# Optimization experiments

Hardware: AMD Instinct MI355X
Metric: run time of the kernel (lower is better)

The kernel has to match this reference:

```python
import jax, jax.numpy as jnp
import numpy as np

NUM_GRAPHS = 128

def setup_inputs() -> dict:
    key = jax.random.key(0)
    k1, k2, k3, k4, k5, k6 = jax.random.split(key, 6)
    N, E, H = 100000, 3200000, 256
    x = jax.random.normal(k1, (N, 1), dtype=jnp.float32)
    edge_index = jax.random.randint(k2, (2, E), 0, N, dtype=jnp.int64)
    batch = jnp.sort(jax.random.randint(k3, (N,), 0, NUM_GRAPHS, dtype=jnp.int64))
    # SAGEConv lin_l: [in=1 -> out=H], plus bias; final Linear [H -> 1]
    W_l = jax.random.normal(k4, (1, H), dtype=jnp.float32) / jnp.sqrt(1.0)
    b_l = jnp.zeros((H,), dtype=jnp.float32)
    W_out = jax.random.normal(k5, (H, 1), dtype=jnp.float32) / jnp.sqrt(H)
    b_out = jax.random.normal(k6, (1,), dtype=jnp.float32) * 0.01
    return {"x": x, "edge_index": edge_index, "batch": batch,
            "W_l": W_l, "b_l": b_l, "W_out": W_out, "b_out": b_out}

def reference(x, edge_index, batch, W_l, b_l, W_out, b_out):
    N = x.shape[0]
    src, dst = edge_index[0], edge_index[1]
    # SAGEConv(aggr='sum', root_weight=False): agg[i] = sum_{j->i} x[j]; out = agg @ W_l + b_l
    agg = jax.ops.segment_sum(x[src], dst, num_segments=N)  # [N,1]
    h = agg @ W_l + b_l                                      # [N,H]
    h = jax.nn.relu(h)
    # global_mean_pool over batch ids
    sums = jax.ops.segment_sum(h, batch, num_segments=NUM_GRAPHS)          # [G,H]
    counts = jax.ops.segment_sum(jnp.ones((N,), h.dtype), batch, num_segments=NUM_GRAPHS)
    pooled = sums / jnp.maximum(counts, 1.0)[:, None]
    out = pooled @ W_out + b_out                             # [G,1]
    return jax.nn.relu(out)
```

## Files before the change

kernel.cpp:

```cpp
#include <hip/hip_runtime.h>


#define GMAX  128
#define HMAX  256
#define BS    256
#define NBMAX 512
#define SG    512
#define BLK2  512
#define CEDGE 6400
#define RSTR  16


__global__ __launch_bounds__(BLK2) void s2_sort(const int* __restrict__ ei,
                                                unsigned* __restrict__ grank,
                                                unsigned* __restrict__ pairs,
                                                int E, int NB, int QpB, int CAP) {
  __shared__ unsigned lp[CEDGE];
  __shared__ unsigned short lb[CEDGE];
  __shared__ unsigned hist[NBMAX];
  __shared__ unsigned sc[NBMAX];
  __shared__ unsigned lbase[NBMAX];
  __shared__ unsigned lrank[NBMAX];
  __shared__ unsigned hb[NBMAX];
  int tid = threadIdx.x, blk = blockIdx.x;

  for (int b = tid; b < NBMAX; b += BLK2) { hist[b] = 0u; lrank[b] = 0u; }
  __syncthreads();

  int Q = E >> 2;
  int q0 = blk * QpB;
  int q1 = min(q0 + QpB, Q);
  const int4* s4 = (const int4*)ei;
  const int4* d4 = (const int4*)(ei + E);

  for (int q = q0 + tid; q < q1; q += BLK2) {
    int4 d = d4[q];
    atomicAdd(&hist[d.x >> 8], 1u);
    atomicAdd(&hist[d.y >> 8], 1u);
    atomicAdd(&hist[d.z >> 8], 1u);
    atomicAdd(&hist[d.w >> 8], 1u);
  }
  if (blk == 0)
    for (int e = (Q << 2) + tid; e < E; e += BLK2)
      atomicAdd(&hist[ei[E + e] >> 8], 1u);
  __syncthreads();

  for (int b = tid; b < NBMAX; b += BLK2) sc[b] = hist[b];
  __syncthreads();
  for (int o = 1; o < NBMAX; o <<= 1) {
    unsigned v = 0u;
    if (tid < NBMAX && tid >= o) v = sc[tid - o];
    __syncthreads();
    if (tid < NBMAX) sc[tid] += v;
    __syncthreads();
  }
  for (int b = tid; b < NB; b += BLK2) {
    unsigned c = hist[b];
    lbase[b] = sc[b] - c;
    unsigned r = c ? atomicAdd(&grank[(size_t)b * RSTR], c) : 0u;
    hb[b] = (unsigned)b * (unsigned)CAP + r;
  }
  __syncthreads();

  for (int q = q0 + tid; q < q1; q += BLK2) {
    int4 s = s4[q];
    int4 d = d4[q];
    { int b = d.x >> 8; unsigned r = atomicAdd(&lrank[b], 1u);
      unsigned p = lbase[b] + r;
      lp[p] = ((unsigned)s.x << 8) | (unsigned)(d.x & 255); lb[p] = (unsigned short)b; }
    { int b = d.y >> 8; unsigned r = atomicAdd(&lrank[b], 1u);
      unsigned p = lbase[b] + r;
      lp[p] = ((unsigned)s.y << 8) | (unsigned)(d.y & 255); lb[p] = (unsigned short)b; }
    { int b = d.z >> 8; unsigned r = atomicAdd(&lrank[b], 1u);
      unsigned p = lbase[b] + r;
      lp[p] = ((unsigned)s.z << 8) | (unsigned)(d.z & 255); lb[p] = (unsigned short)b; }
    { int b = d.w >> 8; unsigned r = atomicAdd(&lrank[b], 1u);
      unsigned p = lbase[b] + r;
      lp[p] = ((unsigned)s.w << 8) | (unsigned)(d.w & 255); lb[p] = (unsigned short)b; }
  }
  int total = (q1 - q0) * 4;
  if (blk == 0) {
    for (int e = (Q << 2) + tid; e < E; e += BLK2) {
      int d = ei[E + e], s = ei[e];
      int b = d >> 8; unsigned r = atomicAdd(&lrank[b], 1u);
      unsigned p = lbase[b] + r;
      lp[p] = ((unsigned)s << 8) | (unsigned)(d & 255); lb[p] = (unsigned short)b;
    }
    total += (E & 3);
  }
  if (total > CEDGE) total = CEDGE;
  __syncthreads();

  unsigned capu = (unsigned)CAP;
  for (int i = tid; i < total; i += BLK2) {
    unsigned b = lb[i];
    unsigned slot = hb[b] + ((unsigned)i - lbase[b]);
    if (slot < (b + 1u) * capu)
      pairs[slot] = lp[i];
  }
}

__global__ __launch_bounds__(1024) void s3_reduce(
    const unsigned* __restrict__ pairs, const unsigned* __restrict__ grank,
    const float* __restrict__ x, const int* __restrict__ batch,
    const float* __restrict__ Wl, const float* __restrict__ bl,
    const float* __restrict__ Wo, const float* __restrict__ b_out,
    float* __restrict__ gsum, float* __restrict__ gcnt,
    unsigned* __restrict__ done, float* __restrict__ out,
    int N, int H, int G, int CAP) {
  __shared__ float acc[BS];
  __shared__ float sWl[HMAX], sbl[HMAX], sWo[HMAX];
  __shared__ float ls[GMAX], lc[GMAX];
  __shared__ unsigned ticket;
  int tid = threadIdx.x, b = blockIdx.x;
  if (tid < BS) acc[tid] = 0.f;
  if (tid < H) { sWl[tid] = Wl[tid]; sbl[tid] = bl[tid]; sWo[tid] = Wo[tid]; }
  if (tid < GMAX) { ls[tid] = 0.f; lc[tid] = 0.f; }
  __syncthreads();

  unsigned lo = (unsigned)b * (unsigned)CAP;
  unsigned cnt = min(grank[(size_t)b * RSTR], (unsigned)CAP);
  unsigned q4 = cnt >> 2;
  const uint4* p4 = (const uint4*)(pairs + lo);
  for (unsigned i = tid; i < q4; i += 1024) {
    uint4 p = p4[i];
    atomicAdd(&acc[p.x & 255u], x[p.x >> 8]);
    atomicAdd(&acc[p.y & 255u], x[p.y >> 8]);
    atomicAdd(&acc[p.z & 255u], x[p.z >> 8]);
    atomicAdd(&acc[p.w & 255u], x[p.w >> 8]);
  }
  if (tid < (int)(cnt & 3u)) {
    unsigned p = pairs[lo + (q4 << 2) + tid];
    atomicAdd(&acc[p & 255u], x[p >> 8]);
  }
  __syncthreads();

  int node = b * BS + tid;
  if (tid < BS && node < N) {
    float a = acc[tid], f = 0.f;
#pragma unroll 8
    for (int k = 0; k < H; ++k) {
      float hh = fmaf(a, sWl[k], sbl[k]);
      f = fmaf(fmaxf(hh, 0.f), sWo[k], f);
    }
    int g = batch[node];
    atomicAdd(&ls[g], f);
    atomicAdd(&lc[g], 1.f);
  }
  __syncthreads();
  if (tid < GMAX && lc[tid] != 0.f) {
    atomicAdd(&gsum[tid], ls[tid]);
    atomicAdd(&gcnt[tid], lc[tid]);
  }
  __syncthreads();
  if (tid == 0)
    ticket = __hip_atomic_fetch_add(done, 1u, __ATOMIC_ACQ_REL,
                                    __HIP_MEMORY_SCOPE_AGENT);
  __syncthreads();
  if (ticket == gridDim.x - 1 && tid < G) {
    float s = __hip_atomic_load(&gsum[tid], __ATOMIC_RELAXED, __HIP_MEMORY_SCOPE_AGENT);
    float c = __hip_atomic_load(&gcnt[tid], __ATOMIC_RELAXED, __HIP_MEMORY_SCOPE_AGENT);
    out[tid] = fmaxf(s / fmaxf(c, 1.f) + b_out[0], 0.f);
  }
}


__global__ __launch_bounds__(256) void fb_scatter(const int* __restrict__ ei,
                                                  const float* __restrict__ x,
                                                  float* __restrict__ agg, int E) {
  int t = blockIdx.x * blockDim.x + threadIdx.x;
  if (t < E) atomicAdd(&agg[ei[E + t]], x[ei[t]]);
}

__global__ __launch_bounds__(256) void fb_node(const float* __restrict__ agg,
                                               const int* __restrict__ batch,
                                               const float* __restrict__ Wl,
                                               const float* __restrict__ bl,
                                               const float* __restrict__ Wo,
                                               float* __restrict__ gsum,
                                               float* __restrict__ gcnt, int N, int H) {
  __shared__ float sWl[HMAX], sbl[HMAX], sWo[HMAX];
  __shared__ float ls[GMAX], lc[GMAX];
  int tid = threadIdx.x;
  if (tid < H) { sWl[tid] = Wl[tid]; sbl[tid] = bl[tid]; sWo[tid] = Wo[tid]; }
  if (tid < GMAX) { ls[tid] = 0.f; lc[tid] = 0.f; }
  __syncthreads();
  int i = blockIdx.x * blockDim.x + tid;
  if (i < N) {
    float a = agg[i], f = 0.f;
    for (int k = 0; k < H; ++k) {
      float hh = fmaf(a, sWl[k], sbl[k]);
      f = fmaf(fmaxf(hh, 0.f), sWo[k], f);
    }
    int g = batch[i];
    atomicAdd(&ls[g], f);
    atomicAdd(&lc[g], 1.f);
  }
  __syncthreads();
  if (tid < GMAX && lc[tid] != 0.f) {
    atomicAdd(&gsum[tid], ls[tid]);
    atomicAdd(&gcnt[tid], lc[tid]);
  }
}

__global__ void fb_final(const float* __restrict__ gsum,
                         const float* __restrict__ gcnt,
                         const float* __restrict__ b_out,
                         float* __restrict__ out, int G) {
  int g = blockIdx.x * blockDim.x + threadIdx.x;
  if (g < G) out[g] = fmaxf(gsum[g] / fmaxf(gcnt[g], 1.f) + b_out[0], 0.f);
}


extern "C" void kernel_launch(void* const* d_in, const int* in_sizes, int n_in,
                              void* d_out, int out_size, void* d_ws, size_t ws_size,
                              hipStream_t stream) {
  const float* x     = (const float*)d_in[0];
  const int*   ei    = (const int*)d_in[1];
  const int*   batch = (const int*)d_in[2];
  const float* Wl    = (const float*)d_in[3];
  const float* bl    = (const float*)d_in[4];
  const float* Wo    = (const float*)d_in[5];
  const float* bo    = (const float*)d_in[6];
  float* out = (float*)d_out;

  int N = in_sizes[0];
  int E = in_sizes[1] / 2;
  int H = in_sizes[3];
  int G = out_size;

  int NB = (N + BS - 1) / BS;
  int Q   = E >> 2;
  int QpB = (Q + SG - 1) / SG;

  int avg = (NB > 0) ? E / NB : 0;
  int CAP = (2 * avg + 4095) & ~4095;
  if (CAP < 4096) CAP = 4096;

  const size_t HDRW = (size_t)NBMAX * RSTR + 2 * GMAX + 4;
  size_t need = (HDRW + (size_t)NB * (size_t)CAP) * 4u;

  unsigned* w = (unsigned*)d_ws;
  if (NB <= NBMAX && ws_size >= need && H <= HMAX && G <= GMAX &&
      QpB * 4 + 4 <= CEDGE) {
    unsigned* grank = w;
    float*    gsum  = (float*)(grank + (size_t)NBMAX * RSTR);
    float*    gcnt  = gsum + GMAX;
    unsigned* done  = (unsigned*)(gcnt + GMAX);
    unsigned* pairs = done + 4;

    hipMemsetAsync(d_ws, 0, HDRW * 4u, stream);
    s2_sort<<<SG, BLK2, 0, stream>>>(ei, grank, pairs, E, NB, QpB, CAP);
    s3_reduce<<<NB, 1024, 0, stream>>>(pairs, grank, x, batch, Wl, bl, Wo, bo,
                                       gsum, gcnt, done, out, N, H, G, CAP);
  } else {
    float* agg  = (float*)d_ws;
    float* gsum = agg + N;
    float* gcnt = gsum + GMAX;
    hipMemsetAsync(d_ws, 0, ((size_t)N + 2 * GMAX) * 4u, stream);
    fb_scatter<<<(E + 255) / 256, 256, 0, stream>>>(ei, x, agg, E);
    fb_node<<<(N + 255) / 256, 256, 0, stream>>>(agg, batch, Wl, bl, Wo,
                                                 gsum, gcnt, N, H);
    fb_final<<<1, 256, 0, stream>>>(gsum, gcnt, bo, out, G);
  }
}
```

Before: 135.8 us.

## Replace bucket-sort aggregation with direct global atomic scatter plus node kernel

Drops the two-pass bucket sort (local histogram, scan, packed pair writes) and shared-memory per-bucket reduction. Edges are now scattered with vectorized int4 loads straight into a global agg array using float atomics, followed by a per-node MLP/pool kernel that keeps the last-block ticket finalize. This removes the pairs write and readback traffic and the sorting work. In exchange, 3.2M edges go through global atomics on random addresses, which may contend or serialize at L2.

```diff
diff --git a/kernel.cpp b/kernel.cpp
--- a/kernel.cpp
+++ b/kernel.cpp
@@ -3,147 +3,53 @@
 
 #define GMAX  128
 #define HMAX  256
-#define BS    256
-#define NBMAX 512
-#define SG    512
-#define BLK2  512
-#define CEDGE 6400
-#define RSTR  16
 
-
-__global__ __launch_bounds__(BLK2) void s2_sort(const int* __restrict__ ei,
-                                                unsigned* __restrict__ grank,
-                                                unsigned* __restrict__ pairs,
-                                                int E, int NB, int QpB, int CAP) {
-  __shared__ unsigned lp[CEDGE];
-  __shared__ unsigned short lb[CEDGE];
-  __shared__ unsigned hist[NBMAX];
-  __shared__ unsigned sc[NBMAX];
-  __shared__ unsigned lbase[NBMAX];
-  __shared__ unsigned lrank[NBMAX];
-  __shared__ unsigned hb[NBMAX];
-  int tid = threadIdx.x, blk = blockIdx.x;
-
-  for (int b = tid; b < NBMAX; b += BLK2) { hist[b] = 0u; lrank[b] = 0u; }
-  __syncthreads();
-
+__global__ __launch_bounds__(256) void e_scatter(const int* __restrict__ ei,
+                                                 const float* __restrict__ x,
+                                                 float* __restrict__ agg, int E) {
   int Q = E >> 2;
-  int q0 = blk * QpB;
-  int q1 = min(q0 + QpB, Q);
   const int4* s4 = (const int4*)ei;
   const int4* d4 = (const int4*)(ei + E);
-
-  for (int q = q0 + tid; q < q1; q += BLK2) {
-    int4 d = d4[q];
-    atomicAdd(&hist[d.x >> 8], 1u);
-    atomicAdd(&hist[d.y >> 8], 1u);
-    atomicAdd(&hist[d.z >> 8], 1u);
-    atomicAdd(&hist[d.w >> 8], 1u);
-  }
-  if (blk == 0)
-    for (int e = (Q << 2) + tid; e < E; e += BLK2)
-      atomicAdd(&hist[ei[E + e] >> 8], 1u);
-  __syncthreads();
-
-  for (int b = tid; b < NBMAX; b += BLK2) sc[b] = hist[b];
-  __syncthreads();
-  for (int o = 1; o < NBMAX; o <<= 1) {
-    unsigned v = 0u;
-    if (tid < NBMAX && tid >= o) v = sc[tid - o];
-    __syncthreads();
-    if (tid < NBMAX) sc[tid] += v;
-    __syncthreads();
-  }
-  for (int b = tid; b < NB; b += BLK2) {
-    unsigned c = hist[b];
-    lbase[b] = sc[b] - c;
-    unsigned r = c ? atomicAdd(&grank[(size_t)b * RSTR], c) : 0u;
-    hb[b] = (unsigned)b * (unsigned)CAP + r;
-  }
-  __syncthreads();
-
-  for (int q = q0 + tid; q < q1; q += BLK2) {
+  int stride = gridDim.x * blockDim.x;
+  for (int q = blockIdx.x * blockDim.x + threadIdx.x; q < Q; q += stride) {
     int4 s = s4[q];
     int4 d = d4[q];
-    { int b = d.x >> 8; unsigned r = atomicAdd(&lrank[b], 1u);
-      unsigned p = lbase[b] + r;
-      lp[p] = ((unsigned)s.x << 8) | (unsigned)(d.x & 255); lb[p] = (unsigned short)b; }
-    { int b = d.y >> 8; unsigned r = atomicAdd(&lrank[b], 1u);
-      unsigned p = lbase[b] + r;
-      lp[p] = ((unsigned)s.y << 8) | (unsigned)(d.y & 255); lb[p] = (unsigned short)b; }
-    { int b = d.z >> 8; unsigned r = atomicAdd(&lrank[b], 1u);
-      unsigned p = lbase[b] + r;
-      lp[p] = ((unsigned)s.z << 8) | (unsigned)(d.z & 255); lb[p] = (unsigned short)b; }
-    { int b = d.w >> 8; unsigned r = atomicAdd(&lrank[b], 1u);
-      unsigned p = lbase[b] + r;
-      lp[p] = ((unsigned)s.w << 8) | (unsigned)(d.w & 255); lb[p] = (unsigned short)b; }
+    float vx = x[s.x], vy = x[s.y], vz = x[s.z], vw = x[s.w];
+    atomicAdd(&agg[d.x], vx);
+    atomicAdd(&agg[d.y], vy);
+    atomicAdd(&agg[d.z], vz);
+    atomicAdd(&agg[d.w], vw);
   }
-  int total = (q1 - q0) * 4;
-  if (blk == 0) {
-    for (int e = (Q << 2) + tid; e < E; e += BLK2) {
-      int d = ei[E + e], s = ei[e];
-      int b = d >> 8; unsigned r = atomicAdd(&lrank[b], 1u);
-      unsigned p = lbase[b] + r;
-      lp[p] = ((unsigned)s << 8) | (unsigned)(d & 255); lb[p] = (unsigned short)b;
-    }
-    total += (E & 3);
-  }
-  if (total > CEDGE) total = CEDGE;
-  __syncthreads();
-
-  unsigned capu = (unsigned)CAP;
-  for (int i = tid; i < total; i += BLK2) {
-    unsigned b = lb[i];
-    unsigned slot = hb[b] + ((unsigned)i - lbase[b]);
-    if (slot < (b + 1u) * capu)
-      pairs[slot] = lp[i];
+  if (blockIdx.x == 0) {
+    for (int e = (Q << 2) + threadIdx.x; e < E; e += 256)
+      atomicAdd(&agg[ei[E + e]], x[ei[e]]);
   }
 }
 
-__global__ __launch_bounds__(1024) void s3_reduce(
-    const unsigned* __restrict__ pairs, const unsigned* __restrict__ grank,
-    const float* __restrict__ x, const int* __restrict__ batch,
+__global__ __launch_bounds__(256) void n_node(
+    const float* __restrict__ agg, const int* __restrict__ batch,
     const float* __restrict__ Wl, const float* __restrict__ bl,
     const float* __restrict__ Wo, const float* __restrict__ b_out,
     float* __restrict__ gsum, float* __restrict__ gcnt,
     unsigned* __restrict__ done, float* __restrict__ out,
-    int N, int H, int G, int CAP) {
-  __shared__ float acc[BS];
+    int N, int H, int G) {
   __shared__ float sWl[HMAX], sbl[HMAX], sWo[HMAX];
   __shared__ float ls[GMAX], lc[GMAX];
   __shared__ unsigned ticket;
-  int tid = threadIdx.x, b = blockIdx.x;
-  if (tid < BS) acc[tid] = 0.f;
+  int tid = threadIdx.x;
   if (tid < H) { sWl[tid] = Wl[tid]; sbl[tid] = bl[tid]; sWo[tid] = Wo[tid]; }
   if (tid < GMAX) { ls[tid] = 0.f; lc[tid] = 0.f; }
   __syncthreads();
 
-  unsigned lo = (unsigned)b * (unsigned)CAP;
-  unsigned cnt = min(grank[(size_t)b * RSTR], (unsigned)CAP);
-  unsigned q4 = cnt >> 2;
-  const uint4* p4 = (const uint4*)(pairs + lo);
-  for (unsigned i = tid; i < q4; i += 1024) {
-    uint4 p = p4[i];
-    atomicAdd(&acc[p.x & 255u], x[p.x >> 8]);
-    atomicAdd(&acc[p.y & 255u], x[p.y >> 8]);
-    atomicAdd(&acc[p.z & 255u], x[p.z >> 8]);
-    atomicAdd(&acc[p.w & 255u], x[p.w >> 8]);
-  }
-  if (tid < (int)(cnt & 3u)) {
-    unsigned p = pairs[lo + (q4 << 2) + tid];
-    atomicAdd(&acc[p & 255u], x[p >> 8]);
-  }
-  __syncthreads();
-
-  int node = b * BS + tid;
-  if (tid < BS && node < N) {
-    float a = acc[tid], f = 0.f;
+  int i = blockIdx.x * blockDim.x + tid;
+  if (i < N) {
+    float a = agg[i], f = 0.f;
 #pragma unroll 8
     for (int k = 0; k < H; ++k) {
       float hh = fmaf(a, sWl[k], sbl[k]);
       f = fmaf(fmaxf(hh, 0.f), sWo[k], f);
     }
-    int g = batch[node];
+    int g = batch[i];
     atomicAdd(&ls[g], f);
     atomicAdd(&lc[g], 1.f);
   }
@@ -165,53 +71,6 @@
 }
 
 
-__global__ __launch_bounds__(256) void fb_scatter(const int* __restrict__ ei,
-                                                  const float* __restrict__ x,
-                                                  float* __restrict__ agg, int E) {
-  int t = blockIdx.x * blockDim.x + threadIdx.x;
-  if (t < E) atomicAdd(&agg[ei[E + t]], x[ei[t]]);
-}
-
-__global__ __launch_bounds__(256) void fb_node(const float* __restrict__ agg,
-                                               const int* __restrict__ batch,
-                                               const float* __restrict__ Wl,
-                                               const float* __restrict__ bl,
-                                               const float* __restrict__ Wo,
-                                               float* __restrict__ gsum,
-                                               float* __restrict__ gcnt, int N, int H) {
-  __shared__ float sWl[HMAX], sbl[HMAX], sWo[HMAX];
-  __shared__ float ls[GMAX], lc[GMAX];
-  int tid = threadIdx.x;
-  if (tid < H) { sWl[tid] = Wl[tid]; sbl[tid] = bl[tid]; sWo[tid] = Wo[tid]; }
-  if (tid < GMAX) { ls[tid] = 0.f; lc[tid] = 0.f; }
-  __syncthreads();
-  int i = blockIdx.x * blockDim.x + tid;
-  if (i < N) {
-    float a = agg[i], f = 0.f;
-    for (int k = 0; k < H; ++k) {
-      float hh = fmaf(a, sWl[k], sbl[k]);
-      f = fmaf(fmaxf(hh, 0.f), sWo[k], f);
-    }
-    int g = batch[i];
-    atomicAdd(&ls[g], f);
-    atomicAdd(&lc[g], 1.f);
-  }
-  __syncthreads();
-  if (tid < GMAX && lc[tid] != 0.f) {
-    atomicAdd(&gsum[tid], ls[tid]);
-    atomicAdd(&gcnt[tid], lc[tid]);
-  }
-}
-
-__global__ void fb_final(const float* __restrict__ gsum,
-                         const float* __restrict__ gcnt,
-                         const float* __restrict__ b_out,
-                         float* __restrict__ out, int G) {
-  int g = blockIdx.x * blockDim.x + threadIdx.x;
-  if (g < G) out[g] = fmaxf(gsum[g] / fmaxf(gcnt[g], 1.f) + b_out[0], 0.f);
-}
-
-
 extern "C" void kernel_launch(void* const* d_in, const int* in_sizes, int n_in,
                               void* d_out, int out_size, void* d_ws, size_t ws_size,
                               hipStream_t stream) {
@@ -229,38 +88,20 @@
   int H = in_sizes[3];
   int G = out_size;
 
-  int NB = (N + BS - 1) / BS;
-  int Q   = E >> 2;
-  int QpB = (Q + SG - 1) / SG;
+  float*    agg  = (float*)d_ws;
+  float*    gsum = agg + N;
+  float*    gcnt = gsum + GMAX;
+  unsigned* done = (unsigned*)(gcnt + GMAX);
 
-  int avg = (NB > 0) ? E / NB : 0;
-  int CAP = (2 * avg + 4095) & ~4095;
-  if (CAP < 4096) CAP = 4096;
+  hipMemsetAsync(d_ws, 0, ((size_t)N + 2 * GMAX + 4) * 4u, stream);
 
-  const size_t HDRW = (size_t)NBMAX * RSTR + 2 * GMAX + 4;
-  size_t need = (HDRW + (size_t)NB * (size_t)CAP) * 4u;
+  int Q = E >> 2;
+  int sg = (Q + 255) / 256;
+  if (sg > 2048) sg = 2048;
+  if (sg < 1) sg = 1;
+  e_scatter<<<sg, 256, 0, stream>>>(ei, x, agg, E);
 
-  unsigned* w = (unsigned*)d_ws;
-  if (NB <= NBMAX && ws_size >= need && H <= HMAX && G <= GMAX &&
-      QpB * 4 + 4 <= CEDGE) {
-    unsigned* grank = w;
-    float*    gsum  = (float*)(grank + (size_t)NBMAX * RSTR);
-    float*    gcnt  = gsum + GMAX;
-    unsigned* done  = (unsigned*)(gcnt + GMAX);
-    unsigned* pairs = done + 4;
-
-    hipMemsetAsync(d_ws, 0, HDRW * 4u, stream);
-    s2_sort<<<SG, BLK2, 0, stream>>>(ei, grank, pairs, E, NB, QpB, CAP);
-    s3_reduce<<<NB, 1024, 0, stream>>>(pairs, grank, x, batch, Wl, bl, Wo, bo,
-                                       gsum, gcnt, done, out, N, H, G, CAP);
-  } else {
-    float* agg  = (float*)d_ws;
-    float* gsum = agg + N;
-    float* gcnt = gsum + GMAX;
-    hipMemsetAsync(d_ws, 0, ((size_t)N + 2 * GMAX) * 4u, stream);
-    fb_scatter<<<(E + 255) / 256, 256, 0, stream>>>(ei, x, agg, E);
-    fb_node<<<(N + 255) / 256, 256, 0, stream>>>(agg, batch, Wl, bl, Wo,
-                                                 gsum, gcnt, N, H);
-    fb_final<<<1, 256, 0, stream>>>(gsum, gcnt, bo, out, G);
-  }
+  int nb = (N + 255) / 256;
+  n_node<<<nb, 256, 0, stream>>>(agg, batch, Wl, bl, Wo, bo,
+                                 gsum, gcnt, done, out, N, H, G);
 }
```

After: 259.1 us. +90.8%, slower.

## Fuse sort and reduce into one cooperative kernel with deterministic bucket offsets

Applied to the files above, without the earlier changes.

Merges the bucketing and reduction kernels into a single cooperative launch that uses grid-wide syncs. Global atomic bucket ranks are replaced by a per-block count matrix whose column prefix sums give each block's offsets. The header zeroing is folded in, which removes the memset. The node MLP loop is split across two half-blocks. This drops two launches and the memset, at the cost of three grid barriers, a hipOccupancy query on every call, and a reduce phase that now runs with 512 threads instead of 1024.

```diff
diff --git a/kernel.cpp b/kernel.cpp
--- a/kernel.cpp
+++ b/kernel.cpp
@@ -1,20 +1,27 @@
 #include <hip/hip_runtime.h>
+#include <hip/hip_cooperative_groups.h>
+
+namespace cg = cooperative_groups;
 
 
 #define GMAX  128
 #define HMAX  256
 #define BS    256
 #define NBMAX 512
-#define SG    512
-#define BLK2  512
+#define NG    512
+#define BLKT  512
 #define CEDGE 6400
-#define RSTR  16
-
-
-__global__ __launch_bounds__(BLK2) void s2_sort(const int* __restrict__ ei,
-                                                unsigned* __restrict__ grank,
-                                                unsigned* __restrict__ pairs,
-                                                int E, int NB, int QpB, int CAP) {
+
+__global__ __launch_bounds__(BLKT, 4) void fused(
+    const int* __restrict__ ei, const float* __restrict__ x,
+    const int* __restrict__ batch, const float* __restrict__ Wl,
+    const float* __restrict__ bl, const float* __restrict__ Wo,
+    const float* __restrict__ bo,
+    unsigned* __restrict__ cnt, unsigned* __restrict__ off,
+    unsigned* __restrict__ tot, float* __restrict__ gsum,
+    float* __restrict__ gcnt, unsigned* __restrict__ done,
+    unsigned* __restrict__ pairs, float* __restrict__ out,
+    int N, int E, int H, int G, int NB, int QpB, int CAP) {
   __shared__ unsigned lp[CEDGE];
   __shared__ unsigned short lb[CEDGE];
   __shared__ unsigned hist[NBMAX];
@@ -22,9 +29,15 @@
   __shared__ unsigned lbase[NBMAX];
   __shared__ unsigned lrank[NBMAX];
   __shared__ unsigned hb[NBMAX];
+  __shared__ float sWl[HMAX], sbl[HMAX], sWo[HMAX];
+  __shared__ float ls[GMAX], lc[GMAX], acc[BS];
+  __shared__ unsigned ticket;
+
+  cg::grid_group grid = cg::this_grid();
   int tid = threadIdx.x, blk = blockIdx.x;
-
-  for (int b = tid; b < NBMAX; b += BLK2) { hist[b] = 0u; lrank[b] = 0u; }
+  int ngrid = (int)gridDim.x;
+
+  for (int b = tid; b < NBMAX; b += BLKT) { hist[b] = 0u; lrank[b] = 0u; }
   __syncthreads();
 
   int Q = E >> 2;
@@ -33,7 +46,7 @@
   const int4* s4 = (const int4*)ei;
   const int4* d4 = (const int4*)(ei + E);
 
-  for (int q = q0 + tid; q < q1; q += BLK2) {
+  for (int q = q0 + tid; q < q1; q += BLKT) {
     int4 d = d4[q];
     atomicAdd(&hist[d.x >> 8], 1u);
     atomicAdd(&hist[d.y >> 8], 1u);
@@ -41,11 +54,11 @@
     atomicAdd(&hist[d.w >> 8], 1u);
   }
   if (blk == 0)
-    for (int e = (Q << 2) + tid; e < E; e += BLK2)
+    for (int e = (Q << 2) + tid; e < E; e += BLKT)
       atomicAdd(&hist[ei[E + e] >> 8], 1u);
   __syncthreads();
 
-  for (int b = tid; b < NBMAX; b += BLK2) sc[b] = hist[b];
+  for (int b = tid; b < NBMAX; b += BLKT) sc[b] = hist[b];
   __syncthreads();
   for (int o = 1; o < NBMAX; o <<= 1) {
     unsigned v = 0u;
@@ -54,15 +67,39 @@
     if (tid < NBMAX) sc[tid] += v;
     __syncthreads();
   }
-  for (int b = tid; b < NB; b += BLK2) {
-    unsigned c = hist[b];
-    lbase[b] = sc[b] - c;
-    unsigned r = c ? atomicAdd(&grank[(size_t)b * RSTR], c) : 0u;
-    hb[b] = (unsigned)b * (unsigned)CAP + r;
-  }
-  __syncthreads();
-
-  for (int q = q0 + tid; q < q1; q += BLK2) {
+  for (int b = tid; b < NBMAX; b += BLKT) lbase[b] = sc[b] - hist[b];
+  for (int b = tid; b < NB; b += BLKT)
+    cnt[(size_t)blk * NBMAX + b] = hist[b];
+  if (blk == ngrid - 1) {
+    if (tid < GMAX) {
+      __hip_atomic_store(&gsum[tid], 0.f, __ATOMIC_RELAXED, __HIP_MEMORY_SCOPE_AGENT);
+      __hip_atomic_store(&gcnt[tid], 0.f, __ATOMIC_RELAXED, __HIP_MEMORY_SCOPE_AGENT);
+    }
+    if (tid == 0)
+      __hip_atomic_store(done, 0u, __ATOMIC_RELAXED, __HIP_MEMORY_SCOPE_AGENT);
+  }
+  grid.sync();
+
+  if (blk < NB) {
+    unsigned c = (tid < ngrid) ? cnt[(size_t)tid * NBMAX + blk] : 0u;
+    sc[tid] = c;
+    __syncthreads();
+    for (int o = 1; o < BLKT; o <<= 1) {
+      unsigned v = (tid >= o) ? sc[tid - o] : 0u;
+      __syncthreads();
+      sc[tid] += v;
+      __syncthreads();
+    }
+    if (tid < ngrid) off[(size_t)tid * NBMAX + blk] = sc[tid] - c;
+    if (tid == BLKT - 1) tot[blk] = sc[tid];
+  }
+  grid.sync();
+
+  for (int b = tid; b < NB; b += BLKT)
+    hb[b] = (unsigned)b * (unsigned)CAP + off[(size_t)blk * NBMAX + b];
+  __syncthreads();
+
+  for (int q = q0 + tid; q < q1; q += BLKT) {
     int4 s = s4[q];
     int4 d = d4[q];
     { int b = d.x >> 8; unsigned r = atomicAdd(&lrank[b], 1u);
@@ -80,7 +117,7 @@
   }
   int total = (q1 - q0) * 4;
   if (blk == 0) {
-    for (int e = (Q << 2) + tid; e < E; e += BLK2) {
+    for (int e = (Q << 2) + tid; e < E; e += BLKT) {
       int d = ei[E + e], s = ei[e];
       int b = d >> 8; unsigned r = atomicAdd(&lrank[b], 1u);
       unsigned p = lbase[b] + r;
@@ -92,60 +129,58 @@
   __syncthreads();
 
   unsigned capu = (unsigned)CAP;
-  for (int i = tid; i < total; i += BLK2) {
+  for (int i = tid; i < total; i += BLKT) {
     unsigned b = lb[i];
     unsigned slot = hb[b] + ((unsigned)i - lbase[b]);
     if (slot < (b + 1u) * capu)
       pairs[slot] = lp[i];
   }
-}
-
-__global__ __launch_bounds__(1024) void s3_reduce(
-    const unsigned* __restrict__ pairs, const unsigned* __restrict__ grank,
-    const float* __restrict__ x, const int* __restrict__ batch,
-    const float* __restrict__ Wl, const float* __restrict__ bl,
-    const float* __restrict__ Wo, const float* __restrict__ b_out,
-    float* __restrict__ gsum, float* __restrict__ gcnt,
-    unsigned* __restrict__ done, float* __restrict__ out,
-    int N, int H, int G, int CAP) {
-  __shared__ float acc[BS];
-  __shared__ float sWl[HMAX], sbl[HMAX], sWo[HMAX];
-  __shared__ float ls[GMAX], lc[GMAX];
-  __shared__ unsigned ticket;
-  int tid = threadIdx.x, b = blockIdx.x;
-  if (tid < BS) acc[tid] = 0.f;
   if (tid < H) { sWl[tid] = Wl[tid]; sbl[tid] = bl[tid]; sWo[tid] = Wo[tid]; }
   if (tid < GMAX) { ls[tid] = 0.f; lc[tid] = 0.f; }
-  __syncthreads();
-
-  unsigned lo = (unsigned)b * (unsigned)CAP;
-  unsigned cnt = min(grank[(size_t)b * RSTR], (unsigned)CAP);
-  unsigned q4 = cnt >> 2;
-  const uint4* p4 = (const uint4*)(pairs + lo);
-  for (unsigned i = tid; i < q4; i += 1024) {
-    uint4 p = p4[i];
-    atomicAdd(&acc[p.x & 255u], x[p.x >> 8]);
-    atomicAdd(&acc[p.y & 255u], x[p.y >> 8]);
-    atomicAdd(&acc[p.z & 255u], x[p.z >> 8]);
-    atomicAdd(&acc[p.w & 255u], x[p.w >> 8]);
-  }
-  if (tid < (int)(cnt & 3u)) {
-    unsigned p = pairs[lo + (q4 << 2) + tid];
-    atomicAdd(&acc[p & 255u], x[p >> 8]);
-  }
-  __syncthreads();
-
-  int node = b * BS + tid;
-  if (tid < BS && node < N) {
-    float a = acc[tid], f = 0.f;
+  if (tid < BS) acc[tid] = 0.f;
+  grid.sync();
+
+  if (blk < NB) {
+    unsigned lo = (unsigned)blk * (unsigned)CAP;
+    unsigned c = min(tot[blk], (unsigned)CAP);
+    unsigned q4 = c >> 2;
+    const uint4* p4 = (const uint4*)(pairs + lo);
+    for (unsigned i = tid; i < q4; i += BLKT) {
+      uint4 p = p4[i];
+      atomicAdd(&acc[p.x & 255u], x[p.x >> 8]);
+      atomicAdd(&acc[p.y & 255u], x[p.y >> 8]);
+      atomicAdd(&acc[p.z & 255u], x[p.z >> 8]);
+      atomicAdd(&acc[p.w & 255u], x[p.w >> 8]);
+    }
+    if (tid < (int)(c & 3u)) {
+      unsigned p = pairs[lo + (q4 << 2) + tid];
+      atomicAdd(&acc[p & 255u], x[p >> 8]);
+    }
+    __syncthreads();
+
+    int half = tid >> 8;
+    int ln = tid & 255;
+    int node = blk * BS + ln;
+    float f = 0.f;
+    if (node < N) {
+      float a = acc[ln];
 #pragma unroll 8
-    for (int k = 0; k < H; ++k) {
-      float hh = fmaf(a, sWl[k], sbl[k]);
-      f = fmaf(fmaxf(hh, 0.f), sWo[k], f);
-    }
-    int g = batch[node];
-    atomicAdd(&ls[g], f);
-    atomicAdd(&lc[g], 1.f);
+      for (int k = half; k < H; k += 2) {
+        float hh = fmaf(a, sWl[k], sbl[k]);
+        f = fmaf(fmaxf(hh, 0.f), sWo[k], f);
+      }
+    }
+    ((float*)sc)[tid] = f;
+    __syncthreads();
+    if (tid < BS) {
+      int nd = blk * BS + tid;
+      if (nd < N) {
+        float ff = ((float*)sc)[tid] + ((float*)sc)[tid + BS];
+        int g = batch[nd];
+        atomicAdd(&ls[g], ff);
+        atomicAdd(&lc[g], 1.f);
+      }
+    }
   }
   __syncthreads();
   if (tid < GMAX && lc[tid] != 0.f) {
@@ -157,10 +192,10 @@
     ticket = __hip_atomic_fetch_add(done, 1u, __ATOMIC_ACQ_REL,
                                     __HIP_MEMORY_SCOPE_AGENT);
   __syncthreads();
-  if (ticket == gridDim.x - 1 && tid < G) {
+  if (ticket == (unsigned)ngrid - 1u && tid < G) {
     float s = __hip_atomic_load(&gsum[tid], __ATOMIC_RELAXED, __HIP_MEMORY_SCOPE_AGENT);
     float c = __hip_atomic_load(&gcnt[tid], __ATOMIC_RELAXED, __HIP_MEMORY_SCOPE_AGENT);
-    out[tid] = fmaxf(s / fmaxf(c, 1.f) + b_out[0], 0.f);
+    out[tid] = fmaxf(s / fmaxf(c, 1.f) + bo[0], 0.f);
   }
 }
 
@@ -231,36 +266,50 @@
 
   int NB = (N + BS - 1) / BS;
   int Q   = E >> 2;
-  int QpB = (Q + SG - 1) / SG;
+  int QpB = (Q + NG - 1) / NG;
 
   int avg = (NB > 0) ? E / NB : 0;
   int CAP = (2 * avg + 4095) & ~4095;
   if (CAP < 4096) CAP = 4096;
 
-  const size_t HDRW = (size_t)NBMAX * RSTR + 2 * GMAX + 4;
+  const size_t W_MAT = (size_t)NG * NBMAX;
+  const size_t HDRW  = 2 * W_MAT + NBMAX + 2 * GMAX + 4;
   size_t need = (HDRW + (size_t)NB * (size_t)CAP) * 4u;
 
-  unsigned* w = (unsigned*)d_ws;
-  if (NB <= NBMAX && ws_size >= need && H <= HMAX && G <= GMAX &&
-      QpB * 4 + 4 <= CEDGE) {
-    unsigned* grank = w;
-    float*    gsum  = (float*)(grank + (size_t)NBMAX * RSTR);
+  int occ = 0;
+  hipError_t oe = hipOccupancyMaxActiveBlocksPerMultiprocessor(&occ, fused, BLKT, 0);
+  bool ok = (oe == hipSuccess) && (occ >= 2) &&
+            NB <= NBMAX && ws_size >= need && H <= HMAX && G <= GMAX &&
+            QpB * 4 + 4 <= CEDGE;
+
+  if (ok) {
+    unsigned* cnt   = (unsigned*)d_ws;
+    unsigned* off   = cnt + W_MAT;
+    unsigned* tot   = off + W_MAT;
+    float*    gsum  = (float*)(tot + NBMAX);
     float*    gcnt  = gsum + GMAX;
     unsigned* done  = (unsigned*)(gcnt + GMAX);
     unsigned* pairs = done + 4;
 
-    hipMemsetAsync(d_ws, 0, HDRW * 4u, stream);
-    s2_sort<<<SG, BLK2, 0, stream>>>(ei, grank, pairs, E, NB, QpB, CAP);
-    s3_reduce<<<NB, 1024, 0, stream>>>(pairs, grank, x, batch, Wl, bl, Wo, bo,
-                                       gsum, gcnt, done, out, N, H, G, CAP);
-  } else {
-    float* agg  = (float*)d_ws;
-    float* gsum = agg + N;
-    float* gcnt = gsum + GMAX;
-    hipMemsetAsync(d_ws, 0, ((size_t)N + 2 * GMAX) * 4u, stream);
-    fb_scatter<<<(E + 255) / 256, 256, 0, stream>>>(ei, x, agg, E);
-    fb_node<<<(N + 255) / 256, 256, 0, stream>>>(agg, batch, Wl, bl, Wo,
-                                                 gsum, gcnt, N, H);
-    fb_final<<<1, 256, 0, stream>>>(gsum, gcnt, bo, out, G);
-  }
-}
+    void* args[] = {(void*)&ei, (void*)&x, (void*)&batch, (void*)&Wl,
+                    (void*)&bl, (void*)&Wo, (void*)&bo,
+                    (void*)&cnt, (void*)&off, (void*)&tot,
+                    (void*)&gsum, (void*)&gcnt, (void*)&done,
+                    (void*)&pairs, (void*)&out,
+                    (void*)&N, (void*)&E, (void*)&H, (void*)&G,
+                    (void*)&NB, (void*)&QpB, (void*)&CAP};
+    hipError_t le = hipLaunchCooperativeKernel((const void*)fused,
+                                               dim3(NG), dim3(BLKT),
+                                               args, 0, stream);
+    if (le == hipSuccess) return;
+  }
+
+  float* agg  = (float*)d_ws;
+  float* gsum = agg + N;
+  float* gcnt = gsum + GMAX;
+  hipMemsetAsync(d_ws, 0, ((size_t)N + 2 * GMAX) * 4u, stream);
+  fb_scatter<<<(E + 255) / 256, 256, 0, stream>>>(ei, x, agg, E);
+  fb_node<<<(N + 255) / 256, 256, 0, stream>>>(agg, batch, Wl, bl, Wo,
+                                               gsum, gcnt, N, H);
+  fb_final<<<1, 256, 0, stream>>>(gsum, gcnt, bo, out, G);
+}
```

Result: slower. 327.6 us (+141.2%).
